# Performance work log

Hardware: AMD Instinct MI355X
Metric: run time of the kernel (lower is better)

Reference implementation:

```python
import jax, jax.numpy as jnp
import numpy as np


def setup_inputs() -> dict:
    key = jax.random.key(0)
    k1, k2 = jax.random.split(key)
    # input: (B, T, C, H, W)
    x = jax.random.normal(k1, (8, 16, 64, 64, 64), dtype=jnp.float32)
    # ConvLSTM gate conv weight: (4*hidden_dim, input_dim + hidden_dim, 3, 3), bias=False
    Wk = jax.random.normal(k2, (256, 128, 3, 3), dtype=jnp.float32) * 0.05
    return {"x": x, "Wk": Wk}


def reference(x, Wk):
    b, t, c, h, w = x.shape
    hd = Wk.shape[0] // 4  # hidden_dim

    def step(carry, xt):
        hid, cell = carry
        z = jnp.concatenate([xt, hid], axis=1)  # (B, C+HD, H, W)
        conv = jax.lax.conv_general_dilated(
            z, Wk, window_strides=(1, 1), padding='SAME',
            dimension_numbers=('NCHW', 'OIHW', 'NCHW'))  # (B, 4*HD, H, W)
        cc_i, cc_f, cc_o, cc_g = jnp.split(conv, 4, axis=1)
        i = jax.nn.sigmoid(cc_i)
        f = jax.nn.sigmoid(cc_f)
        o = jax.nn.sigmoid(cc_o)
        g = jnp.tanh(cc_g)
        cell = f * cell + i * g
        hid = o * jnp.tanh(cell)
        return (hid, cell), None

    h0 = jnp.zeros((b, hd, h, w), dtype=x.dtype)
    c0 = jnp.zeros_like(h0)
    (hid, cell), _ = jax.lax.scan(step, (h0, c0), jnp.swapaxes(x, 0, 1))
    return hid, cell
```

## Files before the change

kernel.cpp:

```cpp
#include <hip/hip_runtime.h>
#include <cmath>


#define CHW 262144

typedef short bf16x8 __attribute__((ext_vector_type(8)));
typedef float f32x4  __attribute__((ext_vector_type(4)));

static __device__ __forceinline__ ushort f2bf(float f) {
    union { float f; unsigned u; } v; v.f = f;
    unsigned u = v.u;
    return (ushort)((u + 0x7FFFu + ((u >> 16) & 1u)) >> 16);
}
static __device__ __forceinline__ float bf2f(ushort u) {
    union { unsigned u; float f; } v; v.u = (unsigned)u << 16; return v.f;
}
static __device__ __forceinline__ float sigf(float x) {
    return 1.f / (1.f + __expf(-x));
}

__global__ void transform_w(const float* __restrict__ Wk, ushort* __restrict__ Wt) {
    const int idx  = blockIdx.x * 256 + threadIdx.x;
    const int lane = idx & 63;
    const int g    = (idx >> 6) & 3;
    const int r2   = idx >> 8;
    const int tap  = r2 % 9;
    const int cq   = r2 / 9;
    const int q    = cq & 3;
    const int cix  = cq >> 2;
    const int oc   = g * 64 + q * 16 + (lane & 15);
    const int icb  = cix * 32 + (lane >> 4) * 8;
    const int ky   = tap / 3, kx = tap - ky * 3;
    ushort* dst = Wt + (size_t)idx * 8;
    #pragma unroll
    for (int j = 0; j < 8; ++j)
        dst[j] = f2bf(Wk[((size_t)(oc * 128 + icb + j) * 3 + ky) * 3 + kx]);
}

__global__ __launch_bounds__(256, 2) void convlstm_step(
    const float*  __restrict__ x,
    const ushort* __restrict__ Wt,
    const ushort* __restrict__ hin,
    ushort*       __restrict__ hout,
    float*        __restrict__ cell,
    int t, int first)
{
    __shared__ __align__(16) ushort zs[324 * 40];
    __shared__ __align__(16) ushort wlds[9 * 4 * 512];

    const int tid  = threadIdx.x;
    const int lane = tid & 63;
    const int w    = tid >> 6;
    const int col  = lane & 15;
    const int quad = lane >> 4;
    const int q8   = quad * 8;

    const int tile = blockIdx.x;
    const int ty0  = (tile >> 2) * 16;
    const int tx0  = (tile & 3) * 16;
    const int q    = blockIdx.y;
    const int hc0  = q * 16;
    const int b    = blockIdx.z;

    const float*  xt = x + ((size_t)b * 16 + t) * CHW;
    const ushort* hb = hin + (size_t)b * CHW;
    float*        cb = cell + (size_t)b * CHW;
    ushort*       ho = hout + (size_t)b * CHW;

    const int gy_ = ty0 + 4 * w;
    const int gx_ = tx0 + quad * 4;

    f32x4 cpv[4];
    #pragma unroll
    for (int r = 0; r < 4; ++r) {
        #pragma unroll
        for (int reg = 0; reg < 4; ++reg) {
            cpv[r][reg] = first ? 0.f
                : cb[((size_t)(gy_ + r) * 64 + gx_ + reg) * 64 + hc0 + col];
        }
    }

    f32x4 acc[4][4];
    #pragma unroll
    for (int r = 0; r < 4; ++r)
        #pragma unroll
        for (int g = 0; g < 4; ++g)
            acc[r][g] = (f32x4){0.f, 0.f, 0.f, 0.f};

    for (int cix = 0; cix < 4; ++cix) {
        __syncthreads();

        {
            const uint4* src = (const uint4*)(Wt + (size_t)(cix * 4 + q) * 18432);
            uint4* dst = (uint4*)wlds;
            #pragma unroll
            for (int k = 0; k < 9; ++k)
                dst[tid + k * 256] = src[tid + k * 256];
        }

        if (cix < 2) {
            #pragma unroll
            for (int k = 0; k < 11; ++k) {
                const int i = tid + k * 256;
                if (i < 2592) {
                    const int icq = i / 324;
                    const int p   = i - icq * 324;
                    const int py  = p / 18;
                    const int px  = p - py * 18;
                    const int gy  = ty0 + py - 1;
                    const int gx  = tx0 + px - 1;
                    const bool inb = ((unsigned)gy < 64u) & ((unsigned)gx < 64u);
                    ushort4 v = {0, 0, 0, 0};
                    if (inb) {
                        const float* src = xt + (size_t)(cix * 32 + icq * 4) * 4096
                                              + gy * 64 + gx;
                        v.x = f2bf(src[0]);
                        v.y = f2bf(src[4096]);
                        v.z = f2bf(src[8192]);
                        v.w = f2bf(src[12288]);
                    }
                    *(ushort4*)&zs[p * 40 + icq * 4] = v;
                }
            }
        } else {
            #pragma unroll
            for (int k = 0; k < 11; ++k) {
                const int i = tid + k * 256;
                if (i < 2592) {
                    const int p   = i >> 3;
                    const int icq = i & 7;
                    const int py  = p / 18;
                    const int px  = p - py * 18;
                    const int gy  = ty0 + py - 1;
                    const int gx  = tx0 + px - 1;
                    const bool inb = ((unsigned)gy < 64u) & ((unsigned)gx < 64u);
                    ushort4 v = {0, 0, 0, 0};
                    if (inb)
                        v = *(const ushort4*)&hb[(size_t)(gy * 64 + gx) * 64
                                                 + (cix - 2) * 32 + icq * 4];
                    *(ushort4*)&zs[p * 40 + icq * 4] = v;
                }
            }
        }
        __syncthreads();

        #pragma unroll
        for (int ky = 0; ky < 3; ++ky) {
            #pragma unroll
            for (int kx = 0; kx < 3; ++kx) {
                const int tap = ky * 3 + kx;
                bf16x8 bfr[4];
                #pragma unroll
                for (int g = 0; g < 4; ++g)
                    bfr[g] = *(const bf16x8*)&wlds[(tap * 4 + g) * 512 + lane * 8];
                bf16x8 av[4];
                #pragma unroll
                for (int r = 0; r < 4; ++r)
                    av[r] = *(const bf16x8*)&zs[((4 * w + r + ky) * 18 + col + kx) * 40 + q8];
                #pragma unroll
                for (int g = 0; g < 4; ++g)
                    #pragma unroll
                    for (int r = 0; r < 4; ++r)
                        acc[r][g] = __builtin_amdgcn_mfma_f32_16x16x32_bf16(
                            av[r], bfr[g], acc[r][g], 0, 0, 0);
            }
        }
    }

    #pragma unroll
    for (int r = 0; r < 4; ++r) {
        const size_t rowbase = ((size_t)(gy_ + r) * 64 + gx_) * 64 + hc0 + col;
        #pragma unroll
        for (int reg = 0; reg < 4; ++reg) {
            const float ci = acc[r][0][reg];
            const float cf = acc[r][1][reg];
            const float co = acc[r][2][reg];
            const float cg = acc[r][3][reg];
            const float cn = sigf(cf) * cpv[r][reg] + sigf(ci) * tanhf(cg);
            const float hn = sigf(co) * tanhf(cn);
            cb[rowbase + (size_t)reg * 64] = cn;
            ho[rowbase + (size_t)reg * 64] = f2bf(hn);
        }
    }
}

__global__ __launch_bounds__(256) void conv_out(
    const ushort* __restrict__ hN, const float* __restrict__ cN,
    float* __restrict__ out)
{
    __shared__ float T[64][65];
    const int tid  = threadIdx.x;
    const int pg   = blockIdx.x;
    const int b    = blockIdx.y;
    const int tsel = blockIdx.z;
    const int pix0 = pg * 64;

    #pragma unroll
    for (int k = 0; k < 16; ++k) {
        const int idx = k * 256 + tid;
        const int pl = idx >> 6, ch = idx & 63;
        const size_t src = (size_t)b * CHW + (size_t)(pix0 + pl) * 64 + ch;
        T[pl][ch] = tsel ? cN[src] : bf2f(hN[src]);
    }
    __syncthreads();
    float* base = out + (tsel ? 2097152 : 0);
    #pragma unroll
    for (int k = 0; k < 16; ++k) {
        const int idx = k * 256 + tid;
        const int ch = idx >> 6, pl = idx & 63;
        base[(size_t)b * CHW + (size_t)ch * 4096 + pix0 + pl] = T[pl][ch];
    }
}

extern "C" void kernel_launch(void* const* d_in, const int* in_sizes, int n_in,
                              void* d_out, int out_size, void* d_ws, size_t ws_size,
                              hipStream_t stream) {
    const float* x  = (const float*)d_in[0];
    const float* Wk = (const float*)d_in[1];
    float* out = (float*)d_out;

    ushort* Wt   = (ushort*)d_ws;
    float*  cellb = (float*)((char*)d_ws + 589824);
    ushort* hb0  = (ushort*)((char*)d_ws + 589824 + 8388608);
    ushort* hb1  = hb0 + 2097152;

    hipMemsetAsync(hb0, 0, 4194304, stream);
    transform_w<<<144, 256, 0, stream>>>(Wk, Wt);

    dim3 grid(16, 4, 8);
    for (int t = 0; t < 16; ++t) {
        const ushort* hi = (t & 1) ? hb1 : hb0;
        ushort*       ho = (t & 1) ? hb0 : hb1;
        convlstm_step<<<grid, 256, 0, stream>>>(x, Wt, hi, ho, cellb, t, t == 0);
    }
    conv_out<<<dim3(64, 8, 2), 256, 0, stream>>>(hb0, cellb, out);
}
```

Before: 889.6 us.

## Fuse all timesteps into one persistent kernel with a grid-wide barrier

Replaces the sixteen per-timestep launches and the output-transpose kernel with one persistent kernel. Blocks sync between timesteps through an atomic counter barrier, keep the cell and hidden state in registers, and prefetch the next x and h chunks into registers while the MFMAs run. Weights are now read straight from global memory (through the cache) instead of being staged in LDS. The kernel writes the NCHW outputs directly at the end. The barrier depends on all 512 blocks being co-resident, and the larger register footprint from the prefetch buffers may limit occupancy or cause spills.

```diff
diff --git a/kernel.cpp b/kernel.cpp
--- a/kernel.cpp
+++ b/kernel.cpp
@@ -2,7 +2,9 @@
 #include <cmath>
 
 
-#define CHW 262144
+#define CHW  262144
+#define NBLK 512
+#define HBUF 2097152
 
 typedef short bf16x8 __attribute__((ext_vector_type(8)));
 typedef float f32x4  __attribute__((ext_vector_type(4)));
@@ -11,9 +13,6 @@
     union { float f; unsigned u; } v; v.f = f;
     unsigned u = v.u;
     return (ushort)((u + 0x7FFFu + ((u >> 16) & 1u)) >> 16);
-}
-static __device__ __forceinline__ float bf2f(ushort u) {
-    union { unsigned u; float f; } v; v.u = (unsigned)u << 16; return v.f;
 }
 static __device__ __forceinline__ float sigf(float x) {
     return 1.f / (1.f + __expf(-x));
@@ -37,16 +36,14 @@
         dst[j] = f2bf(Wk[((size_t)(oc * 128 + icb + j) * 3 + ky) * 3 + kx]);
 }
 
-__global__ __launch_bounds__(256, 2) void convlstm_step(
+__global__ __launch_bounds__(256, 2) void convlstm_all(
     const float*  __restrict__ x,
     const ushort* __restrict__ Wt,
-    const ushort* __restrict__ hin,
-    ushort*       __restrict__ hout,
-    float*        __restrict__ cell,
-    int t, int first)
+    ushort*       __restrict__ hb,
+    float*        __restrict__ out,
+    unsigned*     __restrict__ bar)
 {
     __shared__ __align__(16) ushort zs[324 * 40];
-    __shared__ __align__(16) ushort wlds[9 * 4 * 512];
 
     const int tid  = threadIdx.x;
     const int lane = tid & 63;
@@ -62,153 +59,246 @@
     const int hc0  = q * 16;
     const int b    = blockIdx.z;
 
-    const float*  xt = x + ((size_t)b * 16 + t) * CHW;
-    const ushort* hb = hin + (size_t)b * CHW;
-    float*        cb = cell + (size_t)b * CHW;
-    ushort*       ho = hout + (size_t)b * CHW;
-
     const int gy_ = ty0 + 4 * w;
     const int gx_ = tx0 + quad * 4;
 
-    f32x4 cpv[4];
+    const ushort* wq = Wt + (size_t)q * 18432;
+
+    f32x4 cellv[4];
+    f32x4 hv[4];
     #pragma unroll
     for (int r = 0; r < 4; ++r) {
-        #pragma unroll
-        for (int reg = 0; reg < 4; ++reg) {
-            cpv[r][reg] = first ? 0.f
-                : cb[((size_t)(gy_ + r) * 64 + gx_ + reg) * 64 + hc0 + col];
-        }
+        cellv[r] = (f32x4){0.f, 0.f, 0.f, 0.f};
+        hv[r]    = (f32x4){0.f, 0.f, 0.f, 0.f};
     }
 
-    f32x4 acc[4][4];
+    float   px4[11][4];
+    ushort4 ph[11];
+
+    {
+        const float* xt = x + ((size_t)b * 16 + 0) * CHW;
+        #pragma unroll
+        for (int k = 0; k < 11; ++k) {
+            const int i = tid + k * 256;
+            px4[k][0] = px4[k][1] = px4[k][2] = px4[k][3] = 0.f;
+            if (i < 2592) {
+                const int icq = i / 324;
+                const int p   = i - icq * 324;
+                const int py  = p / 18;
+                const int pxl = p - py * 18;
+                const int gy  = ty0 + py - 1;
+                const int gx  = tx0 + pxl - 1;
+                if (((unsigned)gy < 64u) & ((unsigned)gx < 64u)) {
+                    const float* s = xt + (size_t)(icq * 4) * 4096 + gy * 64 + gx;
+                    px4[k][0] = s[0];
+                    px4[k][1] = s[4096];
+                    px4[k][2] = s[8192];
+                    px4[k][3] = s[12288];
+                }
+            }
+        }
+    }
+
+    for (int t = 0; t < 16; ++t) {
+        const ushort* hin = hb + (size_t)(t & 1) * HBUF + (size_t)b * CHW;
+        ushort*       ho  = hb + (size_t)((t + 1) & 1) * HBUF + (size_t)b * CHW;
+        const float*  xt  = x + ((size_t)b * 16 + t) * CHW;
+
+        f32x4 acc[4][4];
+        #pragma unroll
+        for (int r = 0; r < 4; ++r)
+            #pragma unroll
+            for (int g = 0; g < 4; ++g)
+                acc[r][g] = (f32x4){0.f, 0.f, 0.f, 0.f};
+
+        #pragma unroll
+        for (int cix = 0; cix < 4; ++cix) {
+            __syncthreads();
+            if (cix < 2) {
+                #pragma unroll
+                for (int k = 0; k < 11; ++k) {
+                    const int i = tid + k * 256;
+                    if (i < 2592) {
+                        const int icq = i / 324;
+                        const int p   = i - icq * 324;
+                        ushort4 v;
+                        v.x = f2bf(px4[k][0]);
+                        v.y = f2bf(px4[k][1]);
+                        v.z = f2bf(px4[k][2]);
+                        v.w = f2bf(px4[k][3]);
+                        *(ushort4*)&zs[p * 40 + icq * 4] = v;
+                    }
+                }
+            } else {
+                #pragma unroll
+                for (int k = 0; k < 11; ++k) {
+                    const int i = tid + k * 256;
+                    if (i < 2592) {
+                        const int p   = i >> 3;
+                        const int icq = i & 7;
+                        *(ushort4*)&zs[p * 40 + icq * 4] = ph[k];
+                    }
+                }
+            }
+            __syncthreads();
+
+            if (cix < 2) {
+                if (cix == 0) {
+                    #pragma unroll
+                    for (int k = 0; k < 11; ++k) {
+                        const int i = tid + k * 256;
+                        px4[k][0] = px4[k][1] = px4[k][2] = px4[k][3] = 0.f;
+                        if (i < 2592) {
+                            const int icq = i / 324;
+                            const int p   = i - icq * 324;
+                            const int py  = p / 18;
+                            const int pxl = p - py * 18;
+                            const int gy  = ty0 + py - 1;
+                            const int gx  = tx0 + pxl - 1;
+                            if (((unsigned)gy < 64u) & ((unsigned)gx < 64u)) {
+                                const float* s = xt + (size_t)(32 + icq * 4) * 4096 + gy * 64 + gx;
+                                px4[k][0] = s[0];
+                                px4[k][1] = s[4096];
+                                px4[k][2] = s[8192];
+                                px4[k][3] = s[12288];
+                            }
+                        }
+                    }
+                } else {
+                    #pragma unroll
+                    for (int k = 0; k < 11; ++k) {
+                        const int i = tid + k * 256;
+                        ph[k] = (ushort4){0, 0, 0, 0};
+                        if (i < 2592) {
+                            const int p   = i >> 3;
+                            const int icq = i & 7;
+                            const int py  = p / 18;
+                            const int pxl = p - py * 18;
+                            const int gy  = ty0 + py - 1;
+                            const int gx  = tx0 + pxl - 1;
+                            if (((unsigned)gy < 64u) & ((unsigned)gx < 64u))
+                                ph[k] = *(const ushort4*)&hin[(size_t)(gy * 64 + gx) * 64 + icq * 4];
+                        }
+                    }
+                }
+            } else if (cix == 2) {
+                #pragma unroll
+                for (int k = 0; k < 11; ++k) {
+                    const int i = tid + k * 256;
+                    ph[k] = (ushort4){0, 0, 0, 0};
+                    if (i < 2592) {
+                        const int p   = i >> 3;
+                        const int icq = i & 7;
+                        const int py  = p / 18;
+                        const int pxl = p - py * 18;
+                        const int gy  = ty0 + py - 1;
+                        const int gx  = tx0 + pxl - 1;
+                        if (((unsigned)gy < 64u) & ((unsigned)gx < 64u))
+                            ph[k] = *(const ushort4*)&hin[(size_t)(gy * 64 + gx) * 64 + 32 + icq * 4];
+                    }
+                }
+            } else if (t < 15) {
+                const float* xn = xt + CHW;
+                #pragma unroll
+                for (int k = 0; k < 11; ++k) {
+                    const int i = tid + k * 256;
+                    px4[k][0] = px4[k][1] = px4[k][2] = px4[k][3] = 0.f;
+                    if (i < 2592) {
+                        const int icq = i / 324;
+                        const int p   = i - icq * 324;
+                        const int py  = p / 18;
+                        const int pxl = p - py * 18;
+                        const int gy  = ty0 + py - 1;
+                        const int gx  = tx0 + pxl - 1;
+                        if (((unsigned)gy < 64u) & ((unsigned)gx < 64u)) {
+                            const float* s = xn + (size_t)(icq * 4) * 4096 + gy * 64 + gx;
+                            px4[k][0] = s[0];
+                            px4[k][1] = s[4096];
+                            px4[k][2] = s[8192];
+                            px4[k][3] = s[12288];
+                        }
+                    }
+                }
+            }
+
+            {
+                const ushort* wb = wq + (size_t)cix * 4 * 18432;
+                #pragma unroll
+                for (int kx = 0; kx < 3; ++kx) {
+                    bf16x8 arow[6];
+                    #pragma unroll
+                    for (int j = 0; j < 6; ++j)
+                        arow[j] = *(const bf16x8*)&zs[((4 * w + j) * 18 + col + kx) * 40 + q8];
+                    #pragma unroll
+                    for (int ky = 0; ky < 3; ++ky) {
+                        const int tap = ky * 3 + kx;
+                        bf16x8 bfr[4];
+                        #pragma unroll
+                        for (int g = 0; g < 4; ++g)
+                            bfr[g] = *(const bf16x8*)(wb + (size_t)tap * 2048 + g * 512 + lane * 8);
+                        #pragma unroll
+                        for (int g = 0; g < 4; ++g)
+                            #pragma unroll
+                            for (int r = 0; r < 4; ++r)
+                                acc[r][g] = __builtin_amdgcn_mfma_f32_16x16x32_bf16(
+                                    arow[r + ky], bfr[g], acc[r][g], 0, 0, 0);
+                    }
+                }
+            }
+        }
+
+        #pragma unroll
+        for (int r = 0; r < 4; ++r) {
+            const size_t rowbase = ((size_t)(gy_ + r) * 64 + gx_) * 64 + hc0 + col;
+            #pragma unroll
+            for (int reg = 0; reg < 4; ++reg) {
+                const float ci = acc[r][0][reg];
+                const float cf = acc[r][1][reg];
+                const float co = acc[r][2][reg];
+                const float cg = acc[r][3][reg];
+                const float cn = sigf(cf) * cellv[r][reg] + sigf(ci) * tanhf(cg);
+                const float hn = sigf(co) * tanhf(cn);
+                cellv[r][reg] = cn;
+                hv[r][reg]    = hn;
+                if (t < 15) ho[rowbase + (size_t)reg * 64] = f2bf(hn);
+            }
+        }
+
+        if (t < 15) {
+            __syncthreads();
+            if (tid == 0) {
+                __threadfence();
+                __hip_atomic_fetch_add(bar, 1u, __ATOMIC_RELEASE, __HIP_MEMORY_SCOPE_AGENT);
+                const unsigned target = (unsigned)NBLK * (unsigned)(t + 1);
+                while (__hip_atomic_load(bar, __ATOMIC_ACQUIRE, __HIP_MEMORY_SCOPE_AGENT) < target)
+                    __builtin_amdgcn_s_sleep(2);
+            }
+            __syncthreads();
+        }
+    }
+
+    float* buf = (float*)zs;
+    __syncthreads();
     #pragma unroll
-    for (int r = 0; r < 4; ++r)
-        #pragma unroll
-        for (int g = 0; g < 4; ++g)
-            acc[r][g] = (f32x4){0.f, 0.f, 0.f, 0.f};
-
-    for (int cix = 0; cix < 4; ++cix) {
+    for (int pass = 0; pass < 2; ++pass) {
+        #pragma unroll
+        for (int r = 0; r < 4; ++r)
+            #pragma unroll
+            for (int reg = 0; reg < 4; ++reg) {
+                const int pix = (4 * w + r) * 16 + quad * 4 + reg;
+                buf[col * 257 + pix] = pass ? cellv[r][reg] : hv[r][reg];
+            }
         __syncthreads();
-
-        {
-            const uint4* src = (const uint4*)(Wt + (size_t)(cix * 4 + q) * 18432);
-            uint4* dst = (uint4*)wlds;
-            #pragma unroll
-            for (int k = 0; k < 9; ++k)
-                dst[tid + k * 256] = src[tid + k * 256];
-        }
-
-        if (cix < 2) {
-            #pragma unroll
-            for (int k = 0; k < 11; ++k) {
-                const int i = tid + k * 256;
-                if (i < 2592) {
-                    const int icq = i / 324;
-                    const int p   = i - icq * 324;
-                    const int py  = p / 18;
-                    const int px  = p - py * 18;
-                    const int gy  = ty0 + py - 1;
-                    const int gx  = tx0 + px - 1;
-                    const bool inb = ((unsigned)gy < 64u) & ((unsigned)gx < 64u);
-                    ushort4 v = {0, 0, 0, 0};
-                    if (inb) {
-                        const float* src = xt + (size_t)(cix * 32 + icq * 4) * 4096
-                                              + gy * 64 + gx;
-                        v.x = f2bf(src[0]);
-                        v.y = f2bf(src[4096]);
-                        v.z = f2bf(src[8192]);
-                        v.w = f2bf(src[12288]);
-                    }
-                    *(ushort4*)&zs[p * 40 + icq * 4] = v;
-                }
-            }
-        } else {
-            #pragma unroll
-            for (int k = 0; k < 11; ++k) {
-                const int i = tid + k * 256;
-                if (i < 2592) {
-                    const int p   = i >> 3;
-                    const int icq = i & 7;
-                    const int py  = p / 18;
-                    const int px  = p - py * 18;
-                    const int gy  = ty0 + py - 1;
-                    const int gx  = tx0 + px - 1;
-                    const bool inb = ((unsigned)gy < 64u) & ((unsigned)gx < 64u);
-                    ushort4 v = {0, 0, 0, 0};
-                    if (inb)
-                        v = *(const ushort4*)&hb[(size_t)(gy * 64 + gx) * 64
-                                                 + (cix - 2) * 32 + icq * 4];
-                    *(ushort4*)&zs[p * 40 + icq * 4] = v;
-                }
-            }
+        float* ob = out + (pass ? 2097152 : 0) + (size_t)b * CHW;
+        #pragma unroll
+        for (int k = 0; k < 16; ++k) {
+            const int item = k * 256 + tid;
+            const int chl = item >> 8;
+            const int pix = item & 255;
+            const int py = pix >> 4, pxl = pix & 15;
+            ob[(size_t)(hc0 + chl) * 4096 + (ty0 + py) * 64 + tx0 + pxl] = buf[chl * 257 + pix];
         }
         __syncthreads();
-
-        #pragma unroll
-        for (int ky = 0; ky < 3; ++ky) {
-            #pragma unroll
-            for (int kx = 0; kx < 3; ++kx) {
-                const int tap = ky * 3 + kx;
-                bf16x8 bfr[4];
-                #pragma unroll
-                for (int g = 0; g < 4; ++g)
-                    bfr[g] = *(const bf16x8*)&wlds[(tap * 4 + g) * 512 + lane * 8];
-                bf16x8 av[4];
-                #pragma unroll
-                for (int r = 0; r < 4; ++r)
-                    av[r] = *(const bf16x8*)&zs[((4 * w + r + ky) * 18 + col + kx) * 40 + q8];
-                #pragma unroll
-                for (int g = 0; g < 4; ++g)
-                    #pragma unroll
-                    for (int r = 0; r < 4; ++r)
-                        acc[r][g] = __builtin_amdgcn_mfma_f32_16x16x32_bf16(
-                            av[r], bfr[g], acc[r][g], 0, 0, 0);
-            }
-        }
-    }
-
-    #pragma unroll
-    for (int r = 0; r < 4; ++r) {
-        const size_t rowbase = ((size_t)(gy_ + r) * 64 + gx_) * 64 + hc0 + col;
-        #pragma unroll
-        for (int reg = 0; reg < 4; ++reg) {
-            const float ci = acc[r][0][reg];
-            const float cf = acc[r][1][reg];
-            const float co = acc[r][2][reg];
-            const float cg = acc[r][3][reg];
-            const float cn = sigf(cf) * cpv[r][reg] + sigf(ci) * tanhf(cg);
-            const float hn = sigf(co) * tanhf(cn);
-            cb[rowbase + (size_t)reg * 64] = cn;
-            ho[rowbase + (size_t)reg * 64] = f2bf(hn);
-        }
-    }
-}
-
-__global__ __launch_bounds__(256) void conv_out(
-    const ushort* __restrict__ hN, const float* __restrict__ cN,
-    float* __restrict__ out)
-{
-    __shared__ float T[64][65];
-    const int tid  = threadIdx.x;
-    const int pg   = blockIdx.x;
-    const int b    = blockIdx.y;
-    const int tsel = blockIdx.z;
-    const int pix0 = pg * 64;
-
-    #pragma unroll
-    for (int k = 0; k < 16; ++k) {
-        const int idx = k * 256 + tid;
-        const int pl = idx >> 6, ch = idx & 63;
-        const size_t src = (size_t)b * CHW + (size_t)(pix0 + pl) * 64 + ch;
-        T[pl][ch] = tsel ? cN[src] : bf2f(hN[src]);
-    }
-    __syncthreads();
-    float* base = out + (tsel ? 2097152 : 0);
-    #pragma unroll
-    for (int k = 0; k < 16; ++k) {
-        const int idx = k * 256 + tid;
-        const int ch = idx >> 6, pl = idx & 63;
-        base[(size_t)b * CHW + (size_t)ch * 4096 + pix0 + pl] = T[pl][ch];
     }
 }
 
@@ -219,19 +309,14 @@
     const float* Wk = (const float*)d_in[1];
     float* out = (float*)d_out;
 
-    ushort* Wt   = (ushort*)d_ws;
-    float*  cellb = (float*)((char*)d_ws + 589824);
-    ushort* hb0  = (ushort*)((char*)d_ws + 589824 + 8388608);
-    ushort* hb1  = hb0 + 2097152;
-
-    hipMemsetAsync(hb0, 0, 4194304, stream);
+    ushort*   Wt  = (ushort*)d_ws;
+    unsigned* bar = (unsigned*)((char*)d_ws + 589824);
+    ushort*   hb  = (ushort*)((char*)d_ws + 1048576);
+
+    (void)hipMemsetAsync(bar, 0, 64, stream);
+    (void)hipMemsetAsync(hb, 0, 4194304, stream);
     transform_w<<<144, 256, 0, stream>>>(Wk, Wt);
 
     dim3 grid(16, 4, 8);
-    for (int t = 0; t < 16; ++t) {
-        const ushort* hi = (t & 1) ? hb1 : hb0;
-        ushort*       ho = (t & 1) ? hb0 : hb1;
-        convlstm_step<<<grid, 256, 0, stream>>>(x, Wt, hi, ho, cellb, t, t == 0);
-    }
-    conv_out<<<dim3(64, 8, 2), 256, 0, stream>>>(hb0, cellb, out);
-}
+    convlstm_all<<<grid, 256, 0, stream>>>(x, Wt, hb, out, bar);
+}
```

After: 3.413 ms. 3.84x slower.

## Pre-convert x to bf16 NHWC, double-buffer input tiles, read weights from global

Applied to the files above, without the earlier changes.

A new pre-pass kernel converts all of x from fp32 NCHW to bf16 channels-last once, so each step stages x with the same vectorized loads it uses for h. The step kernel now double-buffers the input halo tile in shared memory, loading the next channel chunk while computing the current one, and drops one barrier per chunk. Weights are read straight from global/L2 instead of being staged in LDS. A row of A fragments is reused across the ky taps. This trades an extra full pass over x plus more global weight traffic for less staging latency and conversion work inside the serial time loop.

```diff
diff --git a/kernel.cpp b/kernel.cpp
--- a/kernel.cpp
+++ b/kernel.cpp
@@ -3,6 +3,7 @@
 
 
 #define CHW 262144
+#define ZSZ 12960
 
 typedef short bf16x8 __attribute__((ext_vector_type(8)));
 typedef float f32x4  __attribute__((ext_vector_type(4)));
@@ -37,16 +38,57 @@
         dst[j] = f2bf(Wk[((size_t)(oc * 128 + icb + j) * 3 + ky) * 3 + kx]);
 }
 
-__global__ __launch_bounds__(256, 2) void convlstm_step(
-    const float*  __restrict__ x,
+__global__ __launch_bounds__(256) void xconv(const float* __restrict__ x,
+                                             ushort* __restrict__ xb) {
+    __shared__ ushort T[256 * 66];
+    const int tid = threadIdx.x;
+    const int pg  = blockIdx.x;
+    const int bt  = blockIdx.y;
+    const float* xt = x  + (size_t)bt * CHW;
+    ushort*      xo = xb + (size_t)bt * CHW;
+    const int p0 = pg * 256;
+    #pragma unroll
+    for (int ch = 0; ch < 64; ++ch)
+        T[tid * 66 + ch] = f2bf(xt[(size_t)ch * 4096 + p0 + tid]);
+    __syncthreads();
+    #pragma unroll
+    for (int k = 0; k < 64; ++k) {
+        const int item = k * 256 + tid;
+        const int px = item >> 6, ch = item & 63;
+        xo[(size_t)(p0 + px) * 64 + ch] = T[px * 66 + ch];
+    }
+}
+
+static __device__ __forceinline__ void stage_chunk(
+    ushort* __restrict__ dst, const ushort* __restrict__ src,
+    int tid, int ty0, int tx0) {
+    #pragma unroll
+    for (int k = 0; k < 11; ++k) {
+        const int i = tid + k * 256;
+        if (i < 2592) {
+            const int p   = i >> 3;
+            const int icq = i & 7;
+            const int py  = p / 18;
+            const int pxl = p - py * 18;
+            const int gy  = ty0 + py - 1;
+            const int gx  = tx0 + pxl - 1;
+            ushort4 v = {0, 0, 0, 0};
+            if (((unsigned)gy < 64u) & ((unsigned)gx < 64u))
+                v = *(const ushort4*)&src[(size_t)(gy * 64 + gx) * 64 + icq * 4];
+            *(ushort4*)&dst[p * 40 + icq * 4] = v;
+        }
+    }
+}
+
+__global__ __launch_bounds__(256) void convlstm_step(
+    const ushort* __restrict__ xb,
     const ushort* __restrict__ Wt,
     const ushort* __restrict__ hin,
     ushort*       __restrict__ hout,
     float*        __restrict__ cell,
     int t, int first)
 {
-    __shared__ __align__(16) ushort zs[324 * 40];
-    __shared__ __align__(16) ushort wlds[9 * 4 * 512];
+    __shared__ __align__(16) ushort zs[2 * ZSZ];
 
     const int tid  = threadIdx.x;
     const int lane = tid & 63;
@@ -62,7 +104,7 @@
     const int hc0  = q * 16;
     const int b    = blockIdx.z;
 
-    const float*  xt = x + ((size_t)b * 16 + t) * CHW;
+    const ushort* xt = xb + ((size_t)b * 16 + t) * CHW;
     const ushort* hb = hin + (size_t)b * CHW;
     float*        cb = cell + (size_t)b * CHW;
     ushort*       ho = hout + (size_t)b * CHW;
@@ -70,15 +112,15 @@
     const int gy_ = ty0 + 4 * w;
     const int gx_ = tx0 + quad * 4;
 
+    const ushort* wq = Wt + (size_t)q * 18432;
+
     f32x4 cpv[4];
     #pragma unroll
-    for (int r = 0; r < 4; ++r) {
-        #pragma unroll
-        for (int reg = 0; reg < 4; ++reg) {
+    for (int r = 0; r < 4; ++r)
+        #pragma unroll
+        for (int reg = 0; reg < 4; ++reg)
             cpv[r][reg] = first ? 0.f
                 : cb[((size_t)(gy_ + r) * 64 + gx_ + reg) * 64 + hc0 + col];
-        }
-    }
 
     f32x4 acc[4][4];
     #pragma unroll
@@ -87,84 +129,41 @@
         for (int g = 0; g < 4; ++g)
             acc[r][g] = (f32x4){0.f, 0.f, 0.f, 0.f};
 
+    stage_chunk(zs, xt, tid, ty0, tx0);
+    __syncthreads();
+
+    #pragma unroll
     for (int cix = 0; cix < 4; ++cix) {
-        __syncthreads();
-
-        {
-            const uint4* src = (const uint4*)(Wt + (size_t)(cix * 4 + q) * 18432);
-            uint4* dst = (uint4*)wlds;
+        ushort* cur = zs + (cix & 1) * ZSZ;
+        ushort* nxt = zs + ((cix + 1) & 1) * ZSZ;
+
+        if (cix == 0) stage_chunk(nxt, xt + 32, tid, ty0, tx0);
+        else if (cix == 1) stage_chunk(nxt, hb, tid, ty0, tx0);
+        else if (cix == 2) stage_chunk(nxt, hb + 32, tid, ty0, tx0);
+
+        const ushort* wb = wq + (size_t)cix * 4 * 18432;
+        #pragma unroll
+        for (int kx = 0; kx < 3; ++kx) {
+            bf16x8 arow[6];
             #pragma unroll
-            for (int k = 0; k < 9; ++k)
-                dst[tid + k * 256] = src[tid + k * 256];
-        }
-
-        if (cix < 2) {
+            for (int j = 0; j < 6; ++j)
+                arow[j] = *(const bf16x8*)&cur[((4 * w + j) * 18 + col + kx) * 40 + q8];
             #pragma unroll
-            for (int k = 0; k < 11; ++k) {
-                const int i = tid + k * 256;
-                if (i < 2592) {
-                    const int icq = i / 324;
-                    const int p   = i - icq * 324;
-                    const int py  = p / 18;
-                    const int px  = p - py * 18;
-                    const int gy  = ty0 + py - 1;
-                    const int gx  = tx0 + px - 1;
-                    const bool inb = ((unsigned)gy < 64u) & ((unsigned)gx < 64u);
-                    ushort4 v = {0, 0, 0, 0};
-                    if (inb) {
-                        const float* src = xt + (size_t)(cix * 32 + icq * 4) * 4096
-                                              + gy * 64 + gx;
-                        v.x = f2bf(src[0]);
-                        v.y = f2bf(src[4096]);
-                        v.z = f2bf(src[8192]);
-                        v.w = f2bf(src[12288]);
-                    }
-                    *(ushort4*)&zs[p * 40 + icq * 4] = v;
-                }
-            }
-        } else {
-            #pragma unroll
-            for (int k = 0; k < 11; ++k) {
-                const int i = tid + k * 256;
-                if (i < 2592) {
-                    const int p   = i >> 3;
-                    const int icq = i & 7;
-                    const int py  = p / 18;
-                    const int px  = p - py * 18;
-                    const int gy  = ty0 + py - 1;
-                    const int gx  = tx0 + px - 1;
-                    const bool inb = ((unsigned)gy < 64u) & ((unsigned)gx < 64u);
-                    ushort4 v = {0, 0, 0, 0};
-                    if (inb)
-                        v = *(const ushort4*)&hb[(size_t)(gy * 64 + gx) * 64
-                                                 + (cix - 2) * 32 + icq * 4];
-                    *(ushort4*)&zs[p * 40 + icq * 4] = v;
-                }
-            }
-        }
-        __syncthreads();
-
-        #pragma unroll
-        for (int ky = 0; ky < 3; ++ky) {
-            #pragma unroll
-            for (int kx = 0; kx < 3; ++kx) {
+            for (int ky = 0; ky < 3; ++ky) {
                 const int tap = ky * 3 + kx;
                 bf16x8 bfr[4];
                 #pragma unroll
                 for (int g = 0; g < 4; ++g)
-                    bfr[g] = *(const bf16x8*)&wlds[(tap * 4 + g) * 512 + lane * 8];
-                bf16x8 av[4];
-                #pragma unroll
-                for (int r = 0; r < 4; ++r)
-                    av[r] = *(const bf16x8*)&zs[((4 * w + r + ky) * 18 + col + kx) * 40 + q8];
+                    bfr[g] = *(const bf16x8*)(wb + (size_t)tap * 2048 + g * 512 + lane * 8);
                 #pragma unroll
                 for (int g = 0; g < 4; ++g)
                     #pragma unroll
                     for (int r = 0; r < 4; ++r)
                         acc[r][g] = __builtin_amdgcn_mfma_f32_16x16x32_bf16(
-                            av[r], bfr[g], acc[r][g], 0, 0, 0);
+                            arow[r + ky], bfr[g], acc[r][g], 0, 0, 0);
             }
         }
+        __syncthreads();
     }
 
     #pragma unroll
@@ -219,19 +218,22 @@
     const float* Wk = (const float*)d_in[1];
     float* out = (float*)d_out;
 
-    ushort* Wt   = (ushort*)d_ws;
-    float*  cellb = (float*)((char*)d_ws + 589824);
-    ushort* hb0  = (ushort*)((char*)d_ws + 589824 + 8388608);
-    ushort* hb1  = hb0 + 2097152;
-
-    hipMemsetAsync(hb0, 0, 4194304, stream);
+    char* ws = (char*)d_ws;
+    ushort* Wt   = (ushort*)ws;
+    float*  cb   = (float*)(ws + (1u << 20));
+    ushort* hb0  = (ushort*)(ws + (16u << 20));
+    ushort* hb1  = (ushort*)(ws + (20u << 20));
+    ushort* xb   = (ushort*)(ws + (32u << 20));
+
+    (void)hipMemsetAsync(hb0, 0, 4194304, stream);
     transform_w<<<144, 256, 0, stream>>>(Wk, Wt);
+    xconv<<<dim3(16, 128), 256, 0, stream>>>(x, xb);
 
     dim3 grid(16, 4, 8);
     for (int t = 0; t < 16; ++t) {
         const ushort* hi = (t & 1) ? hb1 : hb0;
         ushort*       ho = (t & 1) ? hb0 : hb1;
-        convlstm_step<<<grid, 256, 0, stream>>>(x, Wt, hi, ho, cellb, t, t == 0);
-    }
-    conv_out<<<dim3(64, 8, 2), 256, 0, stream>>>(hb0, cellb, out);
-}
+        convlstm_step<<<grid, 256, 0, stream>>>(xb, Wt, hi, ho, cb, t, t == 0);
+    }
+    conv_out<<<dim3(64, 8, 2), 256, 0, stream>>>(hb0, cb, out);
+}
```

Result: faster. 713.5 us (-19.8%).
